# Performance work log

Measured on AMD Instinct MI355X. Metric: run time of the kernel, lower is better.

The kernel has to match this reference:

```python
import jax, jax.numpy as jnp
import numpy as np
from jax import lax

B, H, W = 8, 56, 56
D_MODEL, D_STATE, D_CONV = 96, 32, 3
EXPAND = 2
D_INNER = EXPAND * D_MODEL            # 192
DT_RANK = (D_MODEL + 15) // 16        # 6 ('auto' rule: ceil(d_model/16))
HEAD_D = D_INNER // DT_RANK           # 32
K = 4                                 # 4 cross-scan directions


def cross_scan(x):
    # x: (b,h,w,c) -> (b, L, 4, c): row-major, col-major, and their reverses
    b, h, w, c = x.shape
    x0 = x.reshape(b, h * w, c)
    x1 = jnp.swapaxes(x, 1, 2).reshape(b, h * w, c)
    return jnp.stack([x0, x1, x0[:, ::-1], x1[:, ::-1]], axis=2)


def cross_merge(ys, h, w):
    # ys: (b, L, 4, c) -> (b, L, c), undoing each direction then summing
    b, L, _, c = ys.shape
    untr = lambda t: jnp.swapaxes(t.reshape(b, w, h, c), 1, 2).reshape(b, L, c)
    return ys[:, :, 0] + untr(ys[:, :, 1]) + ys[:, :, 2][:, ::-1] + untr(ys[:, :, 3][:, ::-1])


def layernorm(x, g, b, eps=1e-5):
    mu = x.mean(-1, keepdims=True)
    var = ((x - mu) ** 2).mean(-1, keepdims=True)
    return (x - mu) * lax.rsqrt(var + eps) * g + b


def _forward(x, in_proj_w, conv_w, conv_b, x_proj_w, Ds, A_logs, dt_bias, ln_g, ln_b, out_proj_w):
    b, h, w, _ = x.shape
    L = h * w
    xz = x @ in_proj_w.T                                 # (b,h,w,2*d_inner)
    xi, z = jnp.split(xz, 2, axis=-1)
    z = jax.nn.silu(z)
    pad = (D_CONV - 1) // 2
    xi = lax.conv_general_dilated(xi, conv_w, (1, 1), [(pad, pad), (pad, pad)],
                                  dimension_numbers=('NHWC', 'HWIO', 'NHWC'),
                                  feature_group_count=D_INNER) + conv_b
    xi = jax.nn.silu(xi)
    # ---- forward_core ----
    xs = cross_scan(xi)                                  # (b,L,K,d_inner)
    x_dbl = jnp.einsum('blkd,kcd->blkc', xs, x_proj_w)   # (b,L,K,R+2N)
    dts = x_dbl[..., :DT_RANK]                           # (b,L,K,R)
    Bs = x_dbl[..., DT_RANK:DT_RANK + D_STATE]           # (b,L,K,N)
    Cs = x_dbl[..., DT_RANK + D_STATE:]                  # (b,L,K,N)
    xs_h = xs.reshape(b, L, K, DT_RANK, HEAD_D)          # heads: (k*R+r) -> group k
    A = -jnp.exp(A_logs)                                 # (K,R)
    dt = jax.nn.softplus(dts + dt_bias)                  # (b,L,K,R)
    dA = jnp.exp(dt * A)                                 # (b,L,K,R)

    def step(state, inp):
        x_t, dA_t, dt_t, B_t, C_t = inp
        # state: (b,K,R,HEAD_D,N)
        state = state * dA_t[..., None, None] + jnp.einsum('bkrd,bkr,bkn->bkrdn', x_t, dt_t, B_t)
        y = jnp.einsum('bkrdn,bkn->bkrd', state, C_t)
        return state, y

    mv = lambda t: jnp.moveaxis(t, 1, 0)
    init = jnp.zeros((b, K, DT_RANK, HEAD_D, D_STATE), xi.dtype)
    _, ys = lax.scan(step, init, (mv(xs_h), mv(dA), mv(dt), mv(Bs), mv(Cs)))
    ys = jnp.moveaxis(ys, 0, 1) + xs_h * Ds              # D skip connection
    y = cross_merge(ys.reshape(b, L, K, D_INNER), h, w)  # (b,L,d_inner)
    y = layernorm(y, ln_g, ln_b).reshape(b, h, w, D_INNER)
    # ---- output path ----
    y = jax.nn.gelu(y, approximate=False)
    return (y * z) @ out_proj_w.T


def setup_inputs():
    ks = jax.random.split(jax.random.key(0), 8)
    s = 0.02
    return {
        'x': jax.random.normal(ks[0], (B, H, W, D_MODEL), jnp.float32),
        'in_proj_w': jax.random.normal(ks[1], (2 * D_INNER, D_MODEL), jnp.float32) * s,
        'conv_w': jax.random.normal(ks[2], (D_CONV, D_CONV, 1, D_INNER), jnp.float32) * s,
        'conv_b': jnp.zeros((D_INNER,), jnp.float32),
        'x_proj_w': jax.random.normal(ks[3], (K, DT_RANK + 2 * D_STATE, D_INNER), jnp.float32) * s,
        'Ds': jnp.ones((K, DT_RANK, HEAD_D), jnp.float32),
        'A_logs': jnp.zeros((K, DT_RANK), jnp.float32),
        'dt_bias': 0.1 * jax.random.uniform(ks[4], (K, DT_RANK), dtype=jnp.float32),
        'ln_g': jnp.ones((D_INNER,), jnp.float32),
        'ln_b': jnp.zeros((D_INNER,), jnp.float32),
        'out_proj_w': jax.random.normal(ks[5], (D_MODEL, D_INNER), jnp.float32) * s,
    }


def reference(x, in_proj_w, conv_w, conv_b, x_proj_w, Ds, A_logs, dt_bias, ln_g, ln_b, out_proj_w):
    return _forward(x, in_proj_w, conv_w, conv_b, x_proj_w, Ds, A_logs, dt_bias, ln_g, ln_b, out_proj_w)
```

## Files before the change

kernel.cpp:

```cpp
#include <hip/hip_runtime.h>


constexpr int DM   = 96;
constexpr int DI   = 192;
constexpr int RK   = 6;
constexpr int NS   = 32;
constexpr int KD   = 4;
constexpr int HW   = 56;
constexpr int LT   = 3136;
constexpr int NB   = 8;
constexpr int NPOS = NB * LT;
constexpr int NC   = 49;
constexpr int CH   = 64;
constexpr int SEQ = NB * KD;
constexpr int ELEM = RK * NS * NS;
constexpr int NO   = 280;
constexpr int NOP  = 288;
constexpr int NI   = 384;

typedef __attribute__((ext_vector_type(8))) __bf16 bf16x8;
typedef __attribute__((ext_vector_type(4))) float f32x4;
typedef __attribute__((ext_vector_type(2))) float f32x2;

__device__ __forceinline__ float siluf(float x) { return x / (1.f + __expf(-x)); }

__device__ __forceinline__ unsigned short f2bf(float f) {
  unsigned int u = __float_as_uint(f);
  u = (u + 0x7fffu + ((u >> 16) & 1u)) >> 16;
  return (unsigned short)u;
}
__device__ __forceinline__ float bf2f(unsigned short h) {
  return __uint_as_float(((unsigned int)h) << 16);
}
__device__ __forceinline__ unsigned int pack2(float a, float b) {
  return (unsigned int)f2bf(a) | ((unsigned int)f2bf(b) << 16);
}
__device__ __forceinline__ int xts(int c, int s) {
  return (s & 7) + 8 * ((s >> 3) ^ ((c >> 1) & 7));
}
__device__ __forceinline__ int xtsb(int c, int sblk) {
  return (sblk ^ ((c >> 1) & 7)) * 8;
}

__global__ __launch_bounds__(256) void k_wiprep(const float* __restrict__ Wi,
                                                unsigned short* __restrict__ Wib) {
  int t = blockIdx.x * 256 + threadIdx.x;
  if (t >= NI * DM) return;
  Wib[t] = f2bf(Wi[t]);
}

__global__ __launch_bounds__(256) void k_wprep(const float* __restrict__ Wp,
                                               unsigned short* __restrict__ Wpb) {
  int t = blockIdx.x * 256 + threadIdx.x;
  if (t >= NOP * DI) return;
  int o = t / DI;
  Wpb[t] = (o < NO) ? f2bf(Wp[t]) : (unsigned short)0;
}

__global__ __launch_bounds__(256) void k_wob(const float* __restrict__ Wo,
                                             unsigned short* __restrict__ Wob) {
  int t = blockIdx.x * 256 + threadIdx.x;
  if (t >= DM * DI) return;
  Wob[t] = f2bf(Wo[t]);
}

__global__ __launch_bounds__(256) void k_inproj(const float* __restrict__ x,
                                                const unsigned short* __restrict__ Wib,
                                                float* __restrict__ xi,
                                                float* __restrict__ zs) {
  int wid = threadIdx.x >> 6;
  int lane = threadIdx.x & 63;
  int pos0 = blockIdx.x * 64 + wid * 16;
  int lrow = lane & 15;
  int lgrp = lane >> 4;
  bf16x8 a[3];
  const float* arow = x + (size_t)(pos0 + lrow) * DM + lgrp * 8;
#pragma unroll
  for (int ks = 0; ks < 3; ks++) {
    f32x4 v0 = *reinterpret_cast<const f32x4*>(arow + ks * 32);
    f32x4 v1 = *reinterpret_cast<const f32x4*>(arow + ks * 32 + 4);
    union { unsigned short us[8]; bf16x8 v; } tmp;
#pragma unroll
    for (int j = 0; j < 4; j++) { tmp.us[j] = f2bf(v0[j]); tmp.us[4 + j] = f2bf(v1[j]); }
    a[ks] = tmp.v;
  }
  f32x4 acc[24];
#pragma unroll
  for (int t = 0; t < 24; t++) acc[t] = (f32x4){0.f, 0.f, 0.f, 0.f};
  const unsigned short* brow = Wib + (size_t)lrow * DM + lgrp * 8;
#pragma unroll
  for (int ks = 0; ks < 3; ks++) {
#pragma unroll
    for (int ot = 0; ot < 24; ot++) {
      bf16x8 bf = *reinterpret_cast<const bf16x8*>(brow + (size_t)ot * 16 * DM + ks * 32);
      acc[ot] = __builtin_amdgcn_mfma_f32_16x16x32_bf16(a[ks], bf, acc[ot], 0, 0, 0);
    }
  }
#pragma unroll
  for (int ot = 0; ot < 24; ot++) {
    int o = ot * 16 + lrow;
#pragma unroll
    for (int r = 0; r < 4; r++) {
      int pos = pos0 + lgrp * 4 + r;
      float v = acc[ot][r];
      if (o < DI) xi[(size_t)pos * DI + o] = v;
      else        zs[(size_t)pos * DI + (o - DI)] = siluf(v);
    }
  }
}

__global__ __launch_bounds__(256) void k_conv(const float* __restrict__ xi,
                                              const float* __restrict__ cw,
                                              const float* __restrict__ cb,
                                              unsigned short* __restrict__ xcb,
                                              unsigned short* __restrict__ xcbT) {
  const int DH = DI / 2;
  int t = blockIdx.x * 256 + threadIdx.x;
  if (t >= NPOS * DH) return;
  int c2 = t % DH;
  int pos = t / DH;
  int p = pos % LT, b = pos / LT;
  int h = p / HW, w = p % HW;
  f32x2 acc = *reinterpret_cast<const f32x2*>(cb + c2 * 2);
  int base = b * LT * DI + c2 * 2;
#pragma unroll
  for (int dh = 0; dh < 3; dh++) {
    int hh = h + dh - 1;
    if (hh < 0 || hh >= HW) continue;
#pragma unroll
    for (int dw = 0; dw < 3; dw++) {
      int ww = w + dw - 1;
      if (ww < 0 || ww >= HW) continue;
      f32x2 wv = *reinterpret_cast<const f32x2*>(cw + (dh * 3 + dw) * DI + c2 * 2);
      f32x2 xv = *reinterpret_cast<const f32x2*>(xi + base + (hh * HW + ww) * DI);
      acc += wv * xv;
    }
  }
  unsigned int v = pack2(siluf(acc[0]), siluf(acc[1]));
  reinterpret_cast<unsigned int*>(xcb)[t] = v;
  int pt = w * HW + h;
  reinterpret_cast<unsigned int*>(xcbT)[(b * LT + pt) * DH + c2] = v;
}

__global__ __launch_bounds__(256) void k_xproj(const unsigned short* __restrict__ xcb,
                                               const unsigned short* __restrict__ Wpb,
                                               const float* __restrict__ dt_bias,
                                               float* __restrict__ dtS,
                                               unsigned short* __restrict__ BsH,
                                               unsigned short* __restrict__ CsH) {
  __shared__ float outT[NOP][17];
  int tid = threadIdx.x;
  int wid = tid >> 6;
  int lane = tid & 63;
  int oh = wid >> 1, kh = wid & 1;
  int pos0 = blockIdx.x * 16;
  int lrow = lane & 15;
  int lgrp = lane >> 4;
  bf16x8 a[3];
  const unsigned short* arow = xcb + (size_t)(pos0 + lrow) * DI + kh * 96 + lgrp * 8;
#pragma unroll
  for (int ks = 0; ks < 3; ks++)
    a[ks] = *reinterpret_cast<const bf16x8*>(arow + ks * 32);
  f32x4 acc[9];
#pragma unroll
  for (int t = 0; t < 9; t++) acc[t] = (f32x4){0.f, 0.f, 0.f, 0.f};
  const unsigned short* brow = Wpb + (size_t)(oh * 144 + lrow) * DI + kh * 96 + lgrp * 8;
#pragma unroll
  for (int ks = 0; ks < 3; ks++) {
#pragma unroll
    for (int ot = 0; ot < 9; ot++) {
      bf16x8 bf = *reinterpret_cast<const bf16x8*>(brow + (size_t)ot * 16 * DI + ks * 32);
      acc[ot] = __builtin_amdgcn_mfma_f32_16x16x32_bf16(a[ks], bf, acc[ot], 0, 0, 0);
    }
  }
  if (kh == 1) {
#pragma unroll
    for (int ot = 0; ot < 9; ot++)
#pragma unroll
      for (int q = 0; q < 4; q++)
        outT[oh * 144 + ot * 16 + lrow][lgrp * 4 + q] = acc[ot][q];
  }
  __syncthreads();
  if (kh == 0) {
#pragma unroll
    for (int ot = 0; ot < 9; ot++)
#pragma unroll
      for (int q = 0; q < 4; q++) {
        int o = oh * 144 + ot * 16 + lrow;
        outT[o][lgrp * 4 + q] += acc[ot][q];
      }
  }
  __syncthreads();
  int b = pos0 / LT;
  int p0 = pos0 - b * LT;
  int posl = tid >> 4, cu = tid & 15;
  int p = p0 + posl;
  int h = p / HW, w2 = p - h * HW;
  int pt = w2 * HW + h;
#pragma unroll
  for (int k = 0; k < KD; k++) {
    int sidx = (k * NB + b) * LT + ((k & 1) ? pt : p);
    int rowB = k * 70 + RK;
    int rowC = k * 70 + RK + NS;
    unsigned int vb = pack2(outT[rowB + 2 * cu][posl], outT[rowB + 2 * cu + 1][posl]);
    reinterpret_cast<unsigned int*>(BsH)[(size_t)sidx * 16 + cu] = vb;
    unsigned int vc = pack2(outT[rowC + 2 * cu][posl], outT[rowC + 2 * cu + 1][posl]);
    reinterpret_cast<unsigned int*>(CsH)[(size_t)sidx * 16 + cu] = vc;
  }
#pragma unroll
  for (int i = 0; i < 2; i++) {
    int idx = i * 256 + tid;
    if (idx < 16 * KD * RK) {
      int pp = idx / (KD * RK), rem = idx % (KD * RK);
      int k = rem / RK, c = rem % RK;
      int pg = p0 + pp;
      int hh = pg / HW, ww = pg - hh * HW;
      int ptg = ww * HW + hh;
      int sidx = (k * NB + b) * LT + ((k & 1) ? ptg : pg);
      float v = outT[k * 70 + c][pp] + dt_bias[k * RK + c];
      float dtv = (v > 20.f) ? v : log1pf(__expf(v));
      dtS[(size_t)sidx * RK + c] = dtv;
    }
  }
}

__global__ __launch_bounds__(384) void k_scanAm(const unsigned short* __restrict__ xcb,
                                                const unsigned short* __restrict__ xcbT,
                                                const float* __restrict__ dtS,
                                                const unsigned short* __restrict__ BsH,
                                                const float* __restrict__ A_logs,
                                                unsigned short* __restrict__ Send,
                                                float* __restrict__ Pend) {
  __shared__ unsigned short XT[DI][64];
  __shared__ unsigned short WB[6][32][72];
  int bi = blockIdx.x;
  int chunk = bi % NC;
  int k = (bi / NC) & 3;
  int b = bi / (NC * KD);
  int seq = b * KD + k;
  int tid = threadIdx.x;
  int wid = tid >> 6;
  int lane = tid & 63;
  int lrow = lane & 15, lgrp = lane >> 4;
  int sb0 = (k * NB + b) * LT;
  int j0 = (k < 2) ? chunk * CH : (LT - 1 - chunk * CH);
  int dj = (k < 2) ? 1 : -1;
  const unsigned int* xs32 = reinterpret_cast<const unsigned int*>(
      ((k & 1) ? xcbT : xcb) + (size_t)b * LT * DI);
#pragma unroll
  for (int it = 0; it < 16; ++it) {
    int idx = it * 384 + tid;
    int s = idx / 96, cu = idx - s * 96;
    unsigned int v = xs32[(size_t)(j0 + s * dj) * 96 + cu];
    int col = xts(2 * cu, s);
    XT[2 * cu][col] = (unsigned short)(v & 0xffff);
    XT[2 * cu + 1][col] = (unsigned short)(v >> 16);
  }
  int r = wid;
  float Ar = -__expf(A_logs[k * RK + r]);
  float dt_l = dtS[(size_t)(sb0 + j0 + lane * dj) * RK + r];
  float Lam = dt_l * Ar;
#pragma unroll
  for (int off = 1; off < 64; off <<= 1) {
    float tv = __shfl_up(Lam, off, 64);
    Lam += (lane >= off) ? tv : 0.f;
  }
  float Lam63 = __shfl(Lam, 63, 64);
  float w = __expf(Lam63 - Lam) * dt_l;
  const unsigned int* brow32 = reinterpret_cast<const unsigned int*>(
      BsH + (size_t)(sb0 + j0 + lane * dj) * NS);
#pragma unroll
  for (int i = 0; i < 16; i++) {
    unsigned int v = brow32[i];
    WB[wid][2 * i][lane]     = f2bf(w * bf2f((unsigned short)(v & 0xffff)));
    WB[wid][2 * i + 1][lane] = f2bf(w * bf2f((unsigned short)(v >> 16)));
  }
  __syncthreads();
  f32x4 acc[2][2];
#pragma unroll
  for (int i = 0; i < 2; i++)
#pragma unroll
    for (int j = 0; j < 2; j++) acc[i][j] = (f32x4){0.f, 0.f, 0.f, 0.f};
#pragma unroll
  for (int ks = 0; ks < 2; ks++) {
#pragma unroll
    for (int dtile = 0; dtile < 2; dtile++) {
      int R = r * 32 + dtile * 16 + lrow;
      bf16x8 av = *reinterpret_cast<const bf16x8*>(&XT[R][xtsb(R, ks * 4 + lgrp)]);
#pragma unroll
      for (int ntile = 0; ntile < 2; ntile++) {
        bf16x8 bv = *reinterpret_cast<const bf16x8*>(&WB[wid][ntile * 16 + lrow][ks * 32 + lgrp * 8]);
        acc[dtile][ntile] = __builtin_amdgcn_mfma_f32_16x16x32_bf16(av, bv, acc[dtile][ntile], 0, 0, 0);
      }
    }
  }
#pragma unroll
  for (int dtile = 0; dtile < 2; dtile++)
#pragma unroll
    for (int ntile = 0; ntile < 2; ntile++)
#pragma unroll
      for (int q = 0; q < 4; q++)
        WB[wid][dtile * 16 + lgrp * 4 + q][ntile * 16 + lrow] = f2bf(acc[dtile][ntile][q]);
  if (lane == 0) Pend[(seq * NC + chunk) * RK + r] = __expf(Lam63);
  __syncthreads();
  unsigned int* dst = reinterpret_cast<unsigned int*>(Send + (size_t)(seq * NC + chunk) * ELEM);
  int e0 = tid * 16;
  int rr = e0 >> 10, dd = (e0 >> 5) & 31, nn = e0 & 31;
  const unsigned int* src = reinterpret_cast<const unsigned int*>(&WB[rr][dd][nn]);
#pragma unroll
  for (int i = 0; i < 8; i++) dst[tid * 8 + i] = src[i];
}

__global__ __launch_bounds__(256) void k_scanB(unsigned int* __restrict__ Send32,
                                               const float* __restrict__ Pend) {
  const int EU = ELEM / 2;
  int bi = blockIdx.x;
  int seq = bi / (EU / 256);
  int u = (bi % (EU / 256)) * 256 + threadIdx.x;
  int r = u >> 9;
  float run0 = 0.f, run1 = 0.f;
  for (int c = 0; c < NC; c++) {
    size_t idx = (size_t)(seq * NC + c) * EU + u;
    unsigned int v = Send32[idx];
    float t0 = bf2f((unsigned short)(v & 0xffff));
    float t1 = bf2f((unsigned short)(v >> 16));
    Send32[idx] = pack2(run0, run1);
    float pe = Pend[(seq * NC + c) * RK + r];
    run0 = run0 * pe + t0;
    run1 = run1 * pe + t1;
  }
}

__global__ __launch_bounds__(384) void k_scanM(const unsigned short* __restrict__ xcb,
                                               const unsigned short* __restrict__ xcbT,
                                               const float* __restrict__ dtS,
                                               const unsigned short* __restrict__ BsH,
                                               const unsigned short* __restrict__ CsH,
                                               const float* __restrict__ A_logs,
                                               const float* __restrict__ Ds,
                                               const unsigned short* __restrict__ Sinit,
                                               unsigned short* __restrict__ ybh) {
  __shared__ unsigned short XT[DI][64];
  __shared__ unsigned short GB[6][32][72];
  int bi = blockIdx.x;
  int chunk = bi % NC;
  int k = (bi / NC) & 3;
  int b = bi / (NC * KD);
  int tid = threadIdx.x;
  int wid = tid >> 6;
  int lane = tid & 63;
  int lrow = lane & 15, lgrp = lane >> 4;
  int sb0 = (k * NB + b) * LT;
  int j0 = (k < 2) ? chunk * CH : (LT - 1 - chunk * CH);
  int dj = (k < 2) ? 1 : -1;
  const unsigned int* xs32 = reinterpret_cast<const unsigned int*>(
      ((k & 1) ? xcbT : xcb) + (size_t)b * LT * DI);
#pragma unroll
  for (int it = 0; it < 16; ++it) {
    int idx = it * 384 + tid;
    int s = idx / 96, cu = idx - s * 96;
    unsigned int v = xs32[(size_t)(j0 + s * dj) * 96 + cu];
    int col = xts(2 * cu, s);
    XT[2 * cu][col] = (unsigned short)(v & 0xffff);
    XT[2 * cu + 1][col] = (unsigned short)(v >> 16);
  }
  __syncthreads();
  int r = wid;
  float Ar = -__expf(A_logs[k * RK + r]);
  float dt_l = dtS[(size_t)(sb0 + j0 + lane * dj) * RK + r];
  float Lam = dt_l * Ar;
#pragma unroll
  for (int off = 1; off < 64; off <<= 1) {
    float tv = __shfl_up(Lam, off, 64);
    Lam += (lane >= off) ? tv : 0.f;
  }
  bf16x8 ct[4], bt[4];
#pragma unroll
  for (int i = 0; i < 4; i++) {
    int row = j0 + (i * 16 + lrow) * dj;
    ct[i] = *reinterpret_cast<const bf16x8*>(CsH + (size_t)(sb0 + row) * NS + lgrp * 8);
    bt[i] = *reinterpret_cast<const bf16x8*>(BsH + (size_t)(sb0 + row) * NS + lgrp * 8);
  }
  const unsigned short* sbase = Sinit + (size_t)((b * KD + k) * NC + chunk) * ELEM + r * NS * NS;
  bf16x8 sf[2];
#pragma unroll
  for (int djt = 0; djt < 2; djt++)
    sf[djt] = *reinterpret_cast<const bf16x8*>(sbase + (djt * 16 + lrow) * NS + lgrp * 8);
  f32x4 yi[4][2];
#pragma unroll
  for (int i = 0; i < 4; i++)
#pragma unroll
    for (int djt = 0; djt < 2; djt++)
      yi[i][djt] = __builtin_amdgcn_mfma_f32_16x16x32_bf16(ct[i], sf[djt],
                       (f32x4){0.f, 0.f, 0.f, 0.f}, 0, 0, 0);
  float dt_s4[4], Lam_s4[4];
#pragma unroll
  for (int j = 0; j < 4; j++) {
    dt_s4[j] = __shfl(dt_l, j * 16 + lrow, 64);
    Lam_s4[j] = __shfl(Lam, j * 16 + lrow, 64);
  }
  float Lam_t[4][4];
#pragma unroll
  for (int i = 0; i < 4; i++)
#pragma unroll
    for (int q = 0; q < 4; q++)
      Lam_t[i][q] = __shfl(Lam, i * 16 + lgrp * 4 + q, 64);
  f32x4 y[4][2];
#pragma unroll
  for (int i = 0; i < 4; i++)
#pragma unroll
    for (int djt = 0; djt < 2; djt++) y[i][djt] = (f32x4){0.f, 0.f, 0.f, 0.f};
#pragma unroll
  for (int h = 0; h < 2; h++) {
    int i0 = h * 2;
    int ncol = h ? 4 : 2;
#pragma unroll
    for (int it = 0; it < 2; it++) {
      int i = i0 + it;
#pragma unroll
      for (int j = 0; j < 4; j++) {
        if (j >= ncol) continue;
        f32x4 g = __builtin_amdgcn_mfma_f32_16x16x32_bf16(ct[i], bt[j],
                      (f32x4){0.f, 0.f, 0.f, 0.f}, 0, 0, 0);
        int s = j * 16 + lrow;
#pragma unroll
        for (int q = 0; q < 4; q++) {
          int t = i * 16 + lgrp * 4 + q;
          float wgt = (t >= s) ? __expf(Lam_t[i][q] - Lam_s4[j]) * dt_s4[j] : 0.f;
          GB[wid][it * 16 + lgrp * 4 + q][s] = f2bf(g[q] * wgt);
        }
      }
    }
    int nks = h ? 2 : 1;
#pragma unroll
    for (int it = 0; it < 2; it++) {
#pragma unroll
      for (int ks = 0; ks < nks; ks++) {
        bf16x8 ga = *reinterpret_cast<const bf16x8*>(&GB[wid][it * 16 + lrow][ks * 32 + lgrp * 8]);
#pragma unroll
        for (int djt = 0; djt < 2; djt++) {
          int R = r * 32 + djt * 16 + lrow;
          bf16x8 xb = *reinterpret_cast<const bf16x8*>(&XT[R][xtsb(R, ks * 4 + lgrp)]);
          y[i0 + it][djt] = __builtin_amdgcn_mfma_f32_16x16x32_bf16(ga, xb, y[i0 + it][djt], 0, 0, 0);
        }
      }
    }
  }
  float Dv[2];
#pragma unroll
  for (int djt = 0; djt < 2; djt++)
    Dv[djt] = Ds[(k * RK + r) * NS + djt * 16 + lrow];
  unsigned short* yb = ybh + (size_t)(k * NB + b) * LT * DI;
#pragma unroll
  for (int i = 0; i < 4; i++) {
#pragma unroll
    for (int q = 0; q < 4; q++) {
      int t = i * 16 + lgrp * 4 + q;
      float eL = __expf(Lam_t[i][q]);
      int jrow = j0 + t * dj;
#pragma unroll
      for (int djt = 0; djt < 2; djt++) {
        int R = r * 32 + djt * 16 + lrow;
        float xv = bf2f(XT[R][xts(R, t)]);
        float val = y[i][djt][q] + eL * yi[i][djt][q] + Dv[djt] * xv;
        yb[(size_t)jrow * DI + R] = f2bf(val);
      }
    }
  }
}

__global__ __launch_bounds__(192) void k_ln(const unsigned short* __restrict__ ybh,
                                            const float* __restrict__ zs,
                                            const float* __restrict__ ln_g,
                                            const float* __restrict__ ln_b,
                                            unsigned short* __restrict__ sub) {
  const int PP = 4;
  int pos0 = blockIdx.x * PP;
  int b = pos0 / LT, p0 = pos0 % LT;
  int h0 = p0 / HW, w0 = p0 % HW;
  int pt0 = w0 * HW + h0;
  int tid = threadIdx.x;
  float v[PP], s1[PP], s2[PP];
#pragma unroll
  for (int q = 0; q < PP; q++) {
    int p = p0 + q;
    int pt = pt0 + q * HW;
    float acc = bf2f(ybh[((size_t)(0 * NB + b) * LT + p) * DI + tid])
              + bf2f(ybh[((size_t)(1 * NB + b) * LT + pt) * DI + tid])
              + bf2f(ybh[((size_t)(2 * NB + b) * LT + p) * DI + tid])
              + bf2f(ybh[((size_t)(3 * NB + b) * LT + pt) * DI + tid]);
    v[q] = acc; s1[q] = acc; s2[q] = acc * acc;
  }
#pragma unroll
  for (int off = 32; off; off >>= 1) {
#pragma unroll
    for (int q = 0; q < PP; q++) {
      s1[q] += __shfl_down(s1[q], off, 64);
      s2[q] += __shfl_down(s2[q], off, 64);
    }
  }
  __shared__ float rs1[3][PP], rs2[3][PP];
  int wave = tid >> 6, lane = tid & 63;
  if (lane == 0) {
#pragma unroll
    for (int q = 0; q < PP; q++) { rs1[wave][q] = s1[q]; rs2[wave][q] = s2[q]; }
  }
  __syncthreads();
  float g = ln_g[tid], be = ln_b[tid];
#pragma unroll
  for (int q = 0; q < PP; q++) {
    float mean = (rs1[0][q] + rs1[1][q] + rs1[2][q]) * (1.f / 192.f);
    float var = (rs2[0][q] + rs2[1][q] + rs2[2][q]) * (1.f / 192.f) - mean * mean;
    float rstd = rsqrtf(var + 1e-5f);
    float t = (v[q] - mean) * rstd * g + be;
    float ge = 0.5f * t * (1.f + erff(t * 0.70710678118f));
    sub[(size_t)(pos0 + q) * DI + tid] = f2bf(ge * zs[(size_t)(pos0 + q) * DI + tid]);
  }
}

__global__ __launch_bounds__(256) void k_oproj(const unsigned short* __restrict__ sub,
                                               const unsigned short* __restrict__ Wob,
                                               float* __restrict__ out) {
  int wid = threadIdx.x >> 6;
  int lane = threadIdx.x & 63;
  int pos0 = blockIdx.x * 64 + wid * 16;
  int lrow = lane & 15;
  int lgrp = lane >> 4;
  bf16x8 a[6];
  const unsigned short* arow = sub + (size_t)(pos0 + lrow) * DI + lgrp * 8;
#pragma unroll
  for (int ks = 0; ks < 6; ks++)
    a[ks] = *reinterpret_cast<const bf16x8*>(arow + ks * 32);
  f32x4 acc[6];
#pragma unroll
  for (int t = 0; t < 6; t++) acc[t] = (f32x4){0.f, 0.f, 0.f, 0.f};
  const unsigned short* brow = Wob + (size_t)lrow * DI + lgrp * 8;
#pragma unroll
  for (int ks = 0; ks < 6; ks++) {
#pragma unroll
    for (int ot = 0; ot < 6; ot++) {
      bf16x8 bf = *reinterpret_cast<const bf16x8*>(brow + (size_t)ot * 16 * DI + ks * 32);
      acc[ot] = __builtin_amdgcn_mfma_f32_16x16x32_bf16(a[ks], bf, acc[ot], 0, 0, 0);
    }
  }
#pragma unroll
  for (int ot = 0; ot < 6; ot++) {
    int o = ot * 16 + lrow;
#pragma unroll
    for (int r = 0; r < 4; r++) {
      int pos = pos0 + lgrp * 4 + r;
      out[(size_t)pos * DM + o] = acc[ot][r];
    }
  }
}

extern "C" void kernel_launch(void* const* d_in, const int* in_sizes, int n_in,
                              void* d_out, int out_size, void* d_ws, size_t ws_size,
                              hipStream_t stream) {
  const float* x       = (const float*)d_in[0];
  const float* Wi      = (const float*)d_in[1];
  const float* cw      = (const float*)d_in[2];
  const float* cb      = (const float*)d_in[3];
  const float* Wp      = (const float*)d_in[4];
  const float* Ds      = (const float*)d_in[5];
  const float* A_logs  = (const float*)d_in[6];
  const float* dt_bias = (const float*)d_in[7];
  const float* ln_g    = (const float*)d_in[8];
  const float* ln_b    = (const float*)d_in[9];
  const float* Wo      = (const float*)d_in[10];
  float* out = (float*)d_out;

  float* ws = (float*)d_ws;
  float* xi    = ws;
  float* zs    = xi + (size_t)NPOS * DI;
  float* dtS   = zs + (size_t)NPOS * DI;
  float* Pend  = dtS + (size_t)NPOS * KD * RK;
  float* WpbF  = Pend + (size_t)SEQ * NC * RK;
  float* WibF  = WpbF + (size_t)NOP * DI / 2;
  float* WobF  = WibF + (size_t)NI * DM / 2;
  unsigned short* BsH  = (unsigned short*)(WobF + (size_t)DM * DI / 2);
  unsigned short* CsH  = BsH + (size_t)NPOS * KD * NS;
  unsigned short* xcb  = CsH + (size_t)NPOS * KD * NS;
  unsigned short* xcbT = xcb + (size_t)NPOS * DI;
  unsigned short* ybh  = xcbT + (size_t)NPOS * DI;
  unsigned short* Send = ybh + (size_t)NPOS * KD * DI;
  unsigned short* sub  = Send + (size_t)SEQ * NC * ELEM;
  unsigned short* Wpb = (unsigned short*)WpbF;
  unsigned short* Wib = (unsigned short*)WibF;
  unsigned short* Wob = (unsigned short*)WobF;

  k_wiprep<<<(NI * DM + 255) / 256, 256, 0, stream>>>(Wi, Wib);
  k_wprep<<<(NOP * DI + 255) / 256, 256, 0, stream>>>(Wp, Wpb);
  k_wob<<<(DM * DI + 255) / 256, 256, 0, stream>>>(Wo, Wob);
  k_inproj<<<NPOS / 64, 256, 0, stream>>>(x, Wib, xi, zs);
  k_conv<<<(NPOS * (DI / 2) + 255) / 256, 256, 0, stream>>>(xi, cw, cb, xcb, xcbT);
  k_xproj<<<NPOS / 16, 256, 0, stream>>>(xcb, Wpb, dt_bias, dtS, BsH, CsH);
  k_scanAm<<<SEQ * NC, 384, 0, stream>>>(xcb, xcbT, dtS, BsH, A_logs, Send, Pend);
  k_scanB<<<SEQ * (ELEM / 512), 256, 0, stream>>>((unsigned int*)Send, Pend);
  k_scanM<<<SEQ * NC, 384, 0, stream>>>(xcb, xcbT, dtS, BsH, CsH, A_logs, Ds, Send, ybh);
  k_ln<<<NPOS / 4, 192, 0, stream>>>(ybh, zs, ln_g, ln_b, sub);
  k_oproj<<<NPOS / 64, 256, 0, stream>>>(sub, Wob, out);
}
```

Baseline: 176.3 us.

## Fuse weight prep kernels, store xi/zs in bf16, fuse LN with out-projection

Merges the three weight-conversion kernels into one launch. Stores the in-projection outputs xi and z as bf16 instead of fp32, halving their write and read traffic in the conv and LN stages. Fuses the layernorm/GELU/gating kernel with the output projection, keeping the gated activations in shared memory and splitting K across waves with a shared-memory reduction. This removes two launches and the intermediate sub buffer, but adds extra bf16 rounding of xi/z before the conv and the gating.

```diff
diff --git a/kernel.cpp b/kernel.cpp
--- a/kernel.cpp
+++ b/kernel.cpp
@@ -42,32 +42,28 @@
   return (sblk ^ ((c >> 1) & 7)) * 8;
 }
 
-__global__ __launch_bounds__(256) void k_wiprep(const float* __restrict__ Wi,
-                                                unsigned short* __restrict__ Wib) {
+__global__ __launch_bounds__(256) void k_prep(const float* __restrict__ Wi,
+                                              const float* __restrict__ Wp,
+                                              const float* __restrict__ Wo,
+                                              unsigned short* __restrict__ Wib,
+                                              unsigned short* __restrict__ Wpb,
+                                              unsigned short* __restrict__ Wob) {
   int t = blockIdx.x * 256 + threadIdx.x;
-  if (t >= NI * DM) return;
-  Wib[t] = f2bf(Wi[t]);
-}
-
-__global__ __launch_bounds__(256) void k_wprep(const float* __restrict__ Wp,
-                                               unsigned short* __restrict__ Wpb) {
-  int t = blockIdx.x * 256 + threadIdx.x;
-  if (t >= NOP * DI) return;
-  int o = t / DI;
-  Wpb[t] = (o < NO) ? f2bf(Wp[t]) : (unsigned short)0;
-}
-
-__global__ __launch_bounds__(256) void k_wob(const float* __restrict__ Wo,
-                                             unsigned short* __restrict__ Wob) {
-  int t = blockIdx.x * 256 + threadIdx.x;
-  if (t >= DM * DI) return;
-  Wob[t] = f2bf(Wo[t]);
+  if (t < NI * DM) { Wib[t] = f2bf(Wi[t]); return; }
+  int t2 = t - NI * DM;
+  if (t2 < NOP * DI) {
+    int o = t2 / DI;
+    Wpb[t2] = (o < NO) ? f2bf(Wp[t2]) : (unsigned short)0;
+    return;
+  }
+  int t3 = t2 - NOP * DI;
+  if (t3 < DM * DI) Wob[t3] = f2bf(Wo[t3]);
 }
 
 __global__ __launch_bounds__(256) void k_inproj(const float* __restrict__ x,
                                                 const unsigned short* __restrict__ Wib,
-                                                float* __restrict__ xi,
-                                                float* __restrict__ zs) {
+                                                unsigned short* __restrict__ xi,
+                                                unsigned short* __restrict__ zs) {
   int wid = threadIdx.x >> 6;
   int lane = threadIdx.x & 63;
   int pos0 = blockIdx.x * 64 + wid * 16;
@@ -103,13 +99,13 @@
     for (int r = 0; r < 4; r++) {
       int pos = pos0 + lgrp * 4 + r;
       float v = acc[ot][r];
-      if (o < DI) xi[(size_t)pos * DI + o] = v;
-      else        zs[(size_t)pos * DI + (o - DI)] = siluf(v);
-    }
-  }
-}
-
-__global__ __launch_bounds__(256) void k_conv(const float* __restrict__ xi,
+      if (o < DI) xi[(size_t)pos * DI + o] = f2bf(v);
+      else        zs[(size_t)pos * DI + (o - DI)] = f2bf(siluf(v));
+    }
+  }
+}
+
+__global__ __launch_bounds__(256) void k_conv(const unsigned short* __restrict__ xi,
                                               const float* __restrict__ cw,
                                               const float* __restrict__ cb,
                                               unsigned short* __restrict__ xcb,
@@ -122,7 +118,8 @@
   int p = pos % LT, b = pos / LT;
   int h = p / HW, w = p % HW;
   f32x2 acc = *reinterpret_cast<const f32x2*>(cb + c2 * 2);
-  int base = b * LT * DI + c2 * 2;
+  const unsigned int* x32 = reinterpret_cast<const unsigned int*>(xi);
+  int base = b * LT * DH + c2;
 #pragma unroll
   for (int dh = 0; dh < 3; dh++) {
     int hh = h + dh - 1;
@@ -132,7 +129,8 @@
       int ww = w + dw - 1;
       if (ww < 0 || ww >= HW) continue;
       f32x2 wv = *reinterpret_cast<const f32x2*>(cw + (dh * 3 + dw) * DI + c2 * 2);
-      f32x2 xv = *reinterpret_cast<const f32x2*>(xi + base + (hh * HW + ww) * DI);
+      unsigned int u = x32[base + (hh * HW + ww) * DH];
+      f32x2 xv = {bf2f((unsigned short)(u & 0xffff)), bf2f((unsigned short)(u >> 16))};
       acc += wv * xv;
     }
   }
@@ -469,87 +467,90 @@
   }
 }
 
-__global__ __launch_bounds__(192) void k_ln(const unsigned short* __restrict__ ybh,
-                                            const float* __restrict__ zs,
-                                            const float* __restrict__ ln_g,
-                                            const float* __restrict__ ln_b,
-                                            unsigned short* __restrict__ sub) {
-  const int PP = 4;
-  int pos0 = blockIdx.x * PP;
+__global__ __launch_bounds__(256) void k_lnop(const unsigned short* __restrict__ ybh,
+                                              const unsigned short* __restrict__ zs,
+                                              const float* __restrict__ ln_g,
+                                              const float* __restrict__ ln_b,
+                                              const unsigned short* __restrict__ Wob,
+                                              float* __restrict__ out) {
+  __shared__ unsigned short su[32][200];
+  __shared__ float red[2][6][64][4];
+  int tid = threadIdx.x;
+  int wid = tid >> 6;
+  int lane = tid & 63;
+  int pos0 = blockIdx.x * 32;
   int b = pos0 / LT, p0 = pos0 % LT;
-  int h0 = p0 / HW, w0 = p0 % HW;
-  int pt0 = w0 * HW + h0;
-  int tid = threadIdx.x;
-  float v[PP], s1[PP], s2[PP];
-#pragma unroll
-  for (int q = 0; q < PP; q++) {
-    int p = p0 + q;
-    int pt = pt0 + q * HW;
-    float acc = bf2f(ybh[((size_t)(0 * NB + b) * LT + p) * DI + tid])
-              + bf2f(ybh[((size_t)(1 * NB + b) * LT + pt) * DI + tid])
-              + bf2f(ybh[((size_t)(2 * NB + b) * LT + p) * DI + tid])
-              + bf2f(ybh[((size_t)(3 * NB + b) * LT + pt) * DI + tid]);
-    v[q] = acc; s1[q] = acc; s2[q] = acc * acc;
-  }
-#pragma unroll
-  for (int off = 32; off; off >>= 1) {
-#pragma unroll
-    for (int q = 0; q < PP; q++) {
-      s1[q] += __shfl_down(s1[q], off, 64);
-      s2[q] += __shfl_down(s2[q], off, 64);
-    }
-  }
-  __shared__ float rs1[3][PP], rs2[3][PP];
-  int wave = tid >> 6, lane = tid & 63;
-  if (lane == 0) {
-#pragma unroll
-    for (int q = 0; q < PP; q++) { rs1[wave][q] = s1[q]; rs2[wave][q] = s2[q]; }
-  }
-  __syncthreads();
-  float g = ln_g[tid], be = ln_b[tid];
-#pragma unroll
-  for (int q = 0; q < PP; q++) {
-    float mean = (rs1[0][q] + rs1[1][q] + rs1[2][q]) * (1.f / 192.f);
-    float var = (rs2[0][q] + rs2[1][q] + rs2[2][q]) * (1.f / 192.f) - mean * mean;
+  float g[3], be[3];
+#pragma unroll
+  for (int j = 0; j < 3; j++) { g[j] = ln_g[lane + 64 * j]; be[j] = ln_b[lane + 64 * j]; }
+#pragma unroll
+  for (int q = 0; q < 8; q++) {
+    int pl = wid * 8 + q;
+    int p = p0 + pl;
+    int h = p / HW, w2 = p - h * HW;
+    int pt = w2 * HW + h;
+    float v[3];
+#pragma unroll
+    for (int j = 0; j < 3; j++) {
+      int c = lane + 64 * j;
+      v[j] = bf2f(ybh[((size_t)(0 * NB + b) * LT + p) * DI + c])
+           + bf2f(ybh[((size_t)(1 * NB + b) * LT + pt) * DI + c])
+           + bf2f(ybh[((size_t)(2 * NB + b) * LT + p) * DI + c])
+           + bf2f(ybh[((size_t)(3 * NB + b) * LT + pt) * DI + c]);
+    }
+    float s1 = v[0] + v[1] + v[2];
+    float s2 = v[0] * v[0] + v[1] * v[1] + v[2] * v[2];
+#pragma unroll
+    for (int off = 32; off; off >>= 1) {
+      s1 += __shfl_xor(s1, off, 64);
+      s2 += __shfl_xor(s2, off, 64);
+    }
+    float mean = s1 * (1.f / 192.f);
+    float var = s2 * (1.f / 192.f) - mean * mean;
     float rstd = rsqrtf(var + 1e-5f);
-    float t = (v[q] - mean) * rstd * g + be;
-    float ge = 0.5f * t * (1.f + erff(t * 0.70710678118f));
-    sub[(size_t)(pos0 + q) * DI + tid] = f2bf(ge * zs[(size_t)(pos0 + q) * DI + tid]);
-  }
-}
-
-__global__ __launch_bounds__(256) void k_oproj(const unsigned short* __restrict__ sub,
-                                               const unsigned short* __restrict__ Wob,
-                                               float* __restrict__ out) {
-  int wid = threadIdx.x >> 6;
-  int lane = threadIdx.x & 63;
-  int pos0 = blockIdx.x * 64 + wid * 16;
-  int lrow = lane & 15;
-  int lgrp = lane >> 4;
-  bf16x8 a[6];
-  const unsigned short* arow = sub + (size_t)(pos0 + lrow) * DI + lgrp * 8;
-#pragma unroll
-  for (int ks = 0; ks < 6; ks++)
-    a[ks] = *reinterpret_cast<const bf16x8*>(arow + ks * 32);
+#pragma unroll
+    for (int j = 0; j < 3; j++) {
+      int c = lane + 64 * j;
+      float t = (v[j] - mean) * rstd * g[j] + be[j];
+      float ge = 0.5f * t * (1.f + erff(t * 0.70710678118f));
+      su[pl][c] = f2bf(ge * bf2f(zs[((size_t)(b * LT + p)) * DI + c]));
+    }
+  }
+  __syncthreads();
+  int pg = wid >> 1, kh = wid & 1;
+  int lrow = lane & 15, lgrp = lane >> 4;
+  bf16x8 a[3];
+#pragma unroll
+  for (int ks = 0; ks < 3; ks++)
+    a[ks] = *reinterpret_cast<const bf16x8*>(&su[pg * 16 + lrow][kh * 96 + ks * 32 + lgrp * 8]);
   f32x4 acc[6];
 #pragma unroll
   for (int t = 0; t < 6; t++) acc[t] = (f32x4){0.f, 0.f, 0.f, 0.f};
-  const unsigned short* brow = Wob + (size_t)lrow * DI + lgrp * 8;
-#pragma unroll
-  for (int ks = 0; ks < 6; ks++) {
+  const unsigned short* brow = Wob + (size_t)lrow * DI + kh * 96 + lgrp * 8;
+#pragma unroll
+  for (int ks = 0; ks < 3; ks++) {
 #pragma unroll
     for (int ot = 0; ot < 6; ot++) {
       bf16x8 bf = *reinterpret_cast<const bf16x8*>(brow + (size_t)ot * 16 * DI + ks * 32);
       acc[ot] = __builtin_amdgcn_mfma_f32_16x16x32_bf16(a[ks], bf, acc[ot], 0, 0, 0);
     }
   }
-#pragma unroll
-  for (int ot = 0; ot < 6; ot++) {
-    int o = ot * 16 + lrow;
-#pragma unroll
-    for (int r = 0; r < 4; r++) {
-      int pos = pos0 + lgrp * 4 + r;
-      out[(size_t)pos * DM + o] = acc[ot][r];
+  if (kh == 1) {
+#pragma unroll
+    for (int ot = 0; ot < 6; ot++)
+#pragma unroll
+      for (int q = 0; q < 4; q++) red[pg][ot][lane][q] = acc[ot][q];
+  }
+  __syncthreads();
+  if (kh == 0) {
+#pragma unroll
+    for (int ot = 0; ot < 6; ot++) {
+      int o = ot * 16 + lrow;
+#pragma unroll
+      for (int q = 0; q < 4; q++) {
+        int pos = pos0 + pg * 16 + lgrp * 4 + q;
+        out[(size_t)pos * DM + o] = acc[ot][q] + red[pg][ot][lane][q];
+      }
     }
   }
 }
@@ -571,33 +572,27 @@
   float* out = (float*)d_out;
 
   float* ws = (float*)d_ws;
-  float* xi    = ws;
-  float* zs    = xi + (size_t)NPOS * DI;
-  float* dtS   = zs + (size_t)NPOS * DI;
+  float* dtS   = ws;
   float* Pend  = dtS + (size_t)NPOS * KD * RK;
-  float* WpbF  = Pend + (size_t)SEQ * NC * RK;
-  float* WibF  = WpbF + (size_t)NOP * DI / 2;
-  float* WobF  = WibF + (size_t)NI * DM / 2;
-  unsigned short* BsH  = (unsigned short*)(WobF + (size_t)DM * DI / 2);
+  unsigned short* Wib  = (unsigned short*)(Pend + (size_t)SEQ * NC * RK);
+  unsigned short* Wpb  = Wib + (size_t)NI * DM;
+  unsigned short* Wob  = Wpb + (size_t)NOP * DI;
+  unsigned short* xi   = Wob + (size_t)DM * DI;
+  unsigned short* zs   = xi + (size_t)NPOS * DI;
+  unsigned short* BsH  = zs + (size_t)NPOS * DI;
   unsigned short* CsH  = BsH + (size_t)NPOS * KD * NS;
   unsigned short* xcb  = CsH + (size_t)NPOS * KD * NS;
   unsigned short* xcbT = xcb + (size_t)NPOS * DI;
   unsigned short* ybh  = xcbT + (size_t)NPOS * DI;
   unsigned short* Send = ybh + (size_t)NPOS * KD * DI;
-  unsigned short* sub  = Send + (size_t)SEQ * NC * ELEM;
-  unsigned short* Wpb = (unsigned short*)WpbF;
-  unsigned short* Wib = (unsigned short*)WibF;
-  unsigned short* Wob = (unsigned short*)WobF;
-
-  k_wiprep<<<(NI * DM + 255) / 256, 256, 0, stream>>>(Wi, Wib);
-  k_wprep<<<(NOP * DI + 255) / 256, 256, 0, stream>>>(Wp, Wpb);
-  k_wob<<<(DM * DI + 255) / 256, 256, 0, stream>>>(Wo, Wob);
+
+  int preptot = NI * DM + NOP * DI + DM * DI;
+  k_prep<<<(preptot + 255) / 256, 256, 0, stream>>>(Wi, Wp, Wo, Wib, Wpb, Wob);
   k_inproj<<<NPOS / 64, 256, 0, stream>>>(x, Wib, xi, zs);
   k_conv<<<(NPOS * (DI / 2) + 255) / 256, 256, 0, stream>>>(xi, cw, cb, xcb, xcbT);
   k_xproj<<<NPOS / 16, 256, 0, stream>>>(xcb, Wpb, dt_bias, dtS, BsH, CsH);
   k_scanAm<<<SEQ * NC, 384, 0, stream>>>(xcb, xcbT, dtS, BsH, A_logs, Send, Pend);
   k_scanB<<<SEQ * (ELEM / 512), 256, 0, stream>>>((unsigned int*)Send, Pend);
   k_scanM<<<SEQ * NC, 384, 0, stream>>>(xcb, xcbT, dtS, BsH, CsH, A_logs, Ds, Send, ybh);
-  k_ln<<<NPOS / 4, 192, 0, stream>>>(ybh, zs, ln_g, ln_b, sub);
-  k_oproj<<<NPOS / 64, 256, 0, stream>>>(sub, Wob, out);
-}
+  k_lnop<<<NPOS / 32, 256, 0, stream>>>(ybh, zs, ln_g, ln_b, Wob, out);
+}
```

Result: faster. 161.8 us (-8.3%).
